# Optimization experiments

Measured on AMD Instinct MI355X. Metric: run time of the kernel, lower is better.

The kernel has to match this reference:

```python
import jax
import jax.numpy as jnp
from jax import lax
import numpy as np

VOCAB = 50000
EMBED = 300
HIDDEN = 256
BATCH = 64
SEQ = 256
FORGET_BIAS = 1.0


def setup_inputs() -> dict:
    key = jax.random.key(0)
    k = jax.random.split(key, 6)
    x_in = jax.random.randint(k[0], (BATCH, SEQ), 0, VOCAB, dtype=jnp.int64)
    embedding = jax.random.normal(k[1], (VOCAB, EMBED), dtype=jnp.float32)
    W0 = jax.random.normal(k[2], (EMBED + HIDDEN, 4 * HIDDEN), dtype=jnp.float32) * 0.05
    b0 = jnp.zeros((4 * HIDDEN,), dtype=jnp.float32)
    W1 = jax.random.normal(k[3], (HIDDEN + HIDDEN, 4 * HIDDEN), dtype=jnp.float32) * 0.05
    b1 = jnp.zeros((4 * HIDDEN,), dtype=jnp.float32)
    return {"x_in": x_in, "embedding": embedding, "W0": W0, "b0": b0, "W1": W1, "b1": b1}


def _lstm_layer(xs, W, b):
    # xs: [B, T, D] -> hidden sequence [B, T, H] (BasicLSTMCell, gate order i,j,f,o)
    B = xs.shape[0]
    H = W.shape[1] // 4

    def step(carry, x_t):
        c, h = carry
        gates = jnp.dot(jnp.concatenate([x_t, h], axis=-1), W) + b  # [B, 4H]
        i, j, f, o = jnp.split(gates, 4, axis=-1)
        new_c = c * jax.nn.sigmoid(f + FORGET_BIAS) + jax.nn.sigmoid(i) * jnp.tanh(j)
        new_h = jnp.tanh(new_c) * jax.nn.sigmoid(o)
        return (new_c, new_h), new_h

    init = (jnp.zeros((B, H), xs.dtype), jnp.zeros((B, H), xs.dtype))
    _, hs = lax.scan(step, init, jnp.swapaxes(xs, 0, 1))  # hs: [T, B, H]
    return jnp.swapaxes(hs, 0, 1)


def reference(x_in, embedding, W0, b0, W1, b1):
    word_vecs = embedding[x_in]                 # [B, T, E] frozen embedding lookup
    h1 = _lstm_layer(word_vecs, W0, b0)         # layer 1
    h2 = _lstm_layer(h1, W1, b1)                # layer 2
    return h2[:, -1, :]                          # output at last timestep [B, H]
```

## Files before the change

### kernel.cpp

```cpp
#include <hip/hip_runtime.h>

#define EMBED   300
#define HIDDEN  256
#define SEQ     256
#define NG      1024
#define EPOCHS  258

typedef __attribute__((ext_vector_type(8))) short  short8;
typedef __attribute__((ext_vector_type(4))) float  f32x4;
typedef __attribute__((ext_vector_type(2))) unsigned long long ull2;

__device__ inline unsigned short f2bf(float f) {
    unsigned u = __builtin_bit_cast(unsigned, f);
    return (unsigned short)((u + 0x7FFFu + ((u >> 16) & 1u)) >> 16);
}
__device__ inline float bf2f(unsigned short h) {
    unsigned u = (unsigned)h << 16;
    return __builtin_bit_cast(float, u);
}
__device__ inline float sigm(float x)  { return 1.0f / (1.0f + __expf(-x)); }
__device__ inline float tanh_(float x) { return 2.0f / (1.0f + __expf(-2.0f * x)) - 1.0f; }
__device__ inline int swzb(int c, int base) { return base ^ (((c >> 1) & 3) << 4); }

__device__ inline unsigned ld32a(const unsigned* p) {
    return __hip_atomic_load(p, __ATOMIC_RELAXED, __HIP_MEMORY_SCOPE_AGENT);
}
__device__ inline void st32a(unsigned* p, unsigned v) {
    __hip_atomic_store(p, v, __ATOMIC_RELAXED, __HIP_MEMORY_SCOPE_AGENT);
}
__device__ inline unsigned long long ld64a(const unsigned long long* p) {
    return __hip_atomic_load(p, __ATOMIC_RELAXED, __HIP_MEMORY_SCOPE_AGENT);
}
__device__ inline void st64a(unsigned long long* p, unsigned long long v) {
    __hip_atomic_store(p, v, __ATOMIC_RELAXED, __HIP_MEMORY_SCOPE_AGENT);
}
__device__ inline float ldf32a(const float* p) {
    return __builtin_bit_cast(float, ld32a((const unsigned*)p));
}
__device__ inline void stf32a(float* p, float v) {
    st32a((unsigned*)p, __builtin_bit_cast(unsigned, v));
}
__device__ inline short8 ldh16(const unsigned short* p) {
    ull2 t;
    t.x = ld64a((const unsigned long long*)p);
    t.y = ld64a((const unsigned long long*)p + 1);
    return __builtin_bit_cast(short8, t);
}

#define MFMA(a, b, c) __builtin_amdgcn_mfma_f32_16x16x32_bf16((a), (b), (c), 0, 0, 0)

template <bool FULL>
__global__ __launch_bounds__(256, 1) void lstm_fused(
    const int*   __restrict__ xin,
    const float* __restrict__ emb,
    const float* __restrict__ W0, const float* __restrict__ b0,
    const float* __restrict__ W1, const float* __restrict__ b1,
    unsigned*       __restrict__ flags,
    unsigned short* __restrict__ h1buf,
    unsigned short* __restrict__ h2buf,
    float*          __restrict__ ring1,
    float*          __restrict__ ring2,
    float*          __restrict__ out)
{
    extern __shared__ unsigned short lds[];
    const int tid = threadIdx.x, bid = blockIdx.x;
    const int w = tid >> 6, lane = tid & 63, l15 = lane & 15, q = lane >> 4;
    const int bbase = w * 16, arow = bbase + l15;

    int role, u0 = 0, hc0 = 0;
    if      (bid < 16) { role = 0; u0 = bid * 16; }
    else if (bid < 32) { role = 1; u0 = (bid - 16) * 16; }
    else if (FULL && bid < 48) { role = 2; u0 = (bid - 32) * 16; }
    else { role = 3; hc0 = (bid - (FULL ? 48 : 32)) * 32; }
    const int u = u0 + l15;

    if (bid < 16)       st64a((unsigned long long*)h1buf + bid * 256 + tid, 0ULL);
    else if (bid < 32)  st64a((unsigned long long*)h2buf + (bid - 16) * 256 + tid, 0ULL);

    short8 bfragR[8][4];
    float  bias_r[4];
    float  biasH[2];

    if (role == 0 || role == 1) {
        const float* Wl = role ? W1 : W0;
        const int    ro = role ? HIDDEN : EMBED;
        #pragma unroll
        for (int s = 0; s < 8; ++s)
            #pragma unroll
            for (int nt = 0; nt < 4; ++nt)
                #pragma unroll
                for (int e2 = 0; e2 < 8; ++e2) {
                    int k = ro + s * 32 + q * 8 + e2;
                    bfragR[s][nt][e2] = (short)f2bf(Wl[(long)k * NG + nt * 256 + u0 + l15]);
                }
    }
    if ((FULL && role == 2) || (!FULL && role == 1)) {
        #pragma unroll
        for (int nt = 0; nt < 4; ++nt) bias_r[nt] = b1[nt * 256 + u0 + l15];
        for (int idx = tid; idx < 8 * 64 * 32; idx += 256) {
            int k = idx >> 6, c = idx & 63;
            int col = (c >> 4) * 256 + u0 + (c & 15);
            int s = k >> 5, kk = k & 31;
            *(unsigned short*)((char*)lds + s * 4096 + swzb(c, c * 64 + kk * 2)) =
                f2bf(W1[(long)k * NG + col]);
        }
    }
    if (role == 3) {
        #pragma unroll
        for (int gi = 0; gi < 2; ++gi) biasH[gi] = b0[hc0 + gi * 16 + l15];
        for (int idx = tid; idx < 20 * 32 * 32; idx += 256) {
            int k = idx >> 5, c = idx & 31;
            int s = k >> 5, kk = k & 31;
            int row = (s >= 10) ? (k - 320) : k;
            float v = W0[(long)row * NG + hc0 + c];
            unsigned short hv = f2bf(v);
            if (s >= 10) hv = f2bf(v - bf2f(hv));
            *(unsigned short*)((char*)lds + s * 2048 + swzb(c, c * 64 + kk * 2)) = hv;
        }
    }
    __syncthreads();

    auto produce = [&](int t) {
        int xid = xin[arow * SEQ + t];
        const float* erow = emb + (long)xid * EMBED;
        short8 ac[10];
        #pragma unroll
        for (int s = 0; s < 10; ++s) {
            int kb = s * 32 + q * 8;
            #pragma unroll
            for (int hh = 0; hh < 2; ++hh) {
                int k4 = kb + hh * 4;
                if (k4 < EMBED) {
                    f32x4 v = *(const f32x4*)(erow + k4);
                    #pragma unroll
                    for (int e2 = 0; e2 < 4; ++e2) ac[s][hh * 4 + e2] = (short)f2bf(v[e2]);
                } else {
                    #pragma unroll
                    for (int e2 = 0; e2 < 4; ++e2) ac[s][hh * 4 + e2] = 0;
                }
            }
        }
        f32x4 accg[2];
        #pragma unroll
        for (int gi = 0; gi < 2; ++gi)
            accg[gi] = (f32x4){biasH[gi], biasH[gi], biasH[gi], biasH[gi]};
        #pragma unroll
        for (int s = 0; s < 20; ++s) {
            short8 a = ac[(s < 10) ? s : s - 10];
            #pragma unroll
            for (int gi = 0; gi < 2; ++gi) {
                int c = gi * 16 + l15;
                short8 b = *(const short8*)((char*)lds + s * 2048 + swzb(c, c * 64 + q * 16));
                accg[gi] = MFMA(a, b, accg[gi]);
            }
        }
        float* dst = ring1 + (long)(t & 3) * (64 * NG);
        #pragma unroll
        for (int gi = 0; gi < 2; ++gi)
            #pragma unroll
            for (int rr = 0; rr < 4; ++rr)
                stf32a(dst + (bbase + q * 4 + rr) * NG + hc0 + gi * 16 + l15, accg[gi][rr]);
    };

    if (role == 3) { produce(0); produce(1); produce(2); }

    bool alive = true;
    auto waitall = [&](unsigned tgt) {
        if (alive && w == 0) {
            int n = 0;
            for (;;) {
                unsigned v0 = ld32a(flags + lane * 16);
                unsigned v1 = 0xFFFFFFFFu;
                if (FULL && lane < 16) v1 = ld32a(flags + (64 + lane) * 16);
                if (__all((v0 >= tgt) && (v1 >= tgt))) break;
                if (++n > (1 << 17)) { alive = false; break; }
            }
        }
        __syncthreads();
    };

    asm volatile("s_waitcnt vmcnt(0)" ::: "memory");
    __syncthreads();
    if (tid == 0) { asm volatile("s_waitcnt vmcnt(0)" ::: "memory"); st32a(flags + bid * 16, 1u); }
    waitall(1u);

    float c4[4] = {0.f, 0.f, 0.f, 0.f};
    f32x4 gnext[4];
    f32x4 accx[4];

    if (role == 0) {
        #pragma unroll
        for (int nt = 0; nt < 4; ++nt)
            #pragma unroll
            for (int rr = 0; rr < 4; ++rr)
                gnext[nt][rr] = ldf32a(ring1 + (bbase + q * 4 + rr) * NG + nt * 256 + u0 + l15);
    }

    for (int e = 0; e < EPOCHS; ++e) {
        const int par_w = e & 1, par_r = (e - 1) & 1;

        const bool do_main = (role == 0 && e <= 255) || (role == 1 && e >= 2);
        if (do_main) {
            const unsigned short* hr = (role == 0 ? h1buf : h2buf) + par_r * 16384;
            f32x4 acc[4];
            if (role == 0) {
                #pragma unroll
                for (int nt = 0; nt < 4; ++nt) acc[nt] = gnext[nt];
            } else if (FULL) {
                const float* g2 = ring2 + (long)((e - 2) & 1) * (64 * NG);
                #pragma unroll
                for (int nt = 0; nt < 4; ++nt)
                    #pragma unroll
                    for (int rr = 0; rr < 4; ++rr)
                        acc[nt][rr] = ldf32a(g2 + (bbase + q * 4 + rr) * NG + nt * 256 + u0 + l15);
            } else {
                #pragma unroll
                for (int nt = 0; nt < 4; ++nt) acc[nt] = accx[nt];
            }
            short8 a8[8];
            #pragma unroll
            for (int s = 0; s < 8; ++s)
                a8[s] = ldh16(hr + arow * HIDDEN + s * 32 + q * 8);
            #pragma unroll
            for (int s = 0; s < 8; ++s)
                #pragma unroll
                for (int nt = 0; nt < 4; ++nt)
                    acc[nt] = MFMA(a8[s], bfragR[s][nt], acc[nt]);
            #pragma unroll
            for (int rr = 0; rr < 4; ++rr) {
                int b = bbase + q * 4 + rr;
                float iv = sigm(acc[0][rr]);
                float jv = tanh_(acc[1][rr]);
                float fv = sigm(acc[2][rr] + 1.0f);
                float ov = sigm(acc[3][rr]);
                float cn = c4[rr] * fv + iv * jv;
                c4[rr] = cn;
                float hn = tanh_(cn) * ov;
                *(unsigned short*)((char*)lds + 32768 + (b * 16 + l15) * 2) = f2bf(hn);
                if (role == 1 && e == 257) out[b * HIDDEN + u] = hn;
            }
        } else if (FULL && role == 2 && e >= 1 && e <= 256) {
            const int t = e - 1;
            const unsigned short* h1r = h1buf + (t & 1) * 16384;
            f32x4 g[4];
            #pragma unroll
            for (int nt = 0; nt < 4; ++nt)
                g[nt] = (f32x4){bias_r[nt], bias_r[nt], bias_r[nt], bias_r[nt]};
            #pragma unroll
            for (int s = 0; s < 8; ++s) {
                short8 a = ldh16(h1r + arow * HIDDEN + s * 32 + q * 8);
                #pragma unroll
                for (int nt = 0; nt < 4; ++nt) {
                    int c = nt * 16 + l15;
                    short8 b = *(const short8*)((char*)lds + s * 4096 + swzb(c, c * 64 + q * 16));
                    g[nt] = MFMA(a, b, g[nt]);
                }
            }
            float* dst = ring2 + (long)(t & 1) * (64 * NG);
            #pragma unroll
            for (int nt = 0; nt < 4; ++nt)
                #pragma unroll
                for (int rr = 0; rr < 4; ++rr)
                    stf32a(dst + (bbase + q * 4 + rr) * NG + nt * 256 + u0 + l15, g[nt][rr]);
        }

        __syncthreads();

        if (do_main) {
            unsigned short* hw = (role == 0 ? h1buf : h2buf) + par_w * 16384;
            unsigned long long v = *(unsigned long long*)((char*)lds + 32768 + tid * 8);
            int r = tid >> 2, p = tid & 3;
            st64a((unsigned long long*)(hw + r * HIDDEN + u0) + p, v);
        }
        asm volatile("s_waitcnt vmcnt(0)" ::: "memory");
        __syncthreads();
        if (tid == 0) { asm volatile("s_waitcnt vmcnt(0)" ::: "memory"); st32a(flags + bid * 16, (unsigned)(e + 2)); }

        if (role == 0 && e + 1 <= 255) {
            const float* g1 = ring1 + (long)((e + 1) & 3) * (64 * NG);
            #pragma unroll
            for (int nt = 0; nt < 4; ++nt)
                #pragma unroll
                for (int rr = 0; rr < 4; ++rr)
                    gnext[nt][rr] = ldf32a(g1 + (bbase + q * 4 + rr) * NG + nt * 256 + u0 + l15);
        } else if (!FULL && role == 1 && e >= 1 && e <= 256) {
            const unsigned short* h1r = h1buf + ((e - 1) & 1) * 16384;
            #pragma unroll
            for (int nt = 0; nt < 4; ++nt)
                accx[nt] = (f32x4){bias_r[nt], bias_r[nt], bias_r[nt], bias_r[nt]};
            #pragma unroll
            for (int s = 0; s < 8; ++s) {
                short8 a = ldh16(h1r + arow * HIDDEN + s * 32 + q * 8);
                #pragma unroll
                for (int nt = 0; nt < 4; ++nt) {
                    int c = nt * 16 + l15;
                    short8 b = *(const short8*)((char*)lds + s * 4096 + swzb(c, c * 64 + q * 16));
                    accx[nt] = MFMA(a, b, accx[nt]);
                }
            }
        } else if (role == 3 && e <= 252) {
            produce(e + 3);
        }

        waitall((unsigned)(e + 2));
    }
}

__global__ void ws_too_small_sentinel(float* out, int n) {
    int i = blockIdx.x * 256 + threadIdx.x;
    if (i < n) out[i] = 31337.0f;
}

extern "C" void kernel_launch(void* const* d_in, const int* in_sizes, int n_in,
                              void* d_out, int out_size, void* d_ws, size_t ws_size,
                              hipStream_t stream)
{
    const int*   xin = (const int*)d_in[0];
    const float* emb = (const float*)d_in[1];
    const float* W0  = (const float*)d_in[2];
    const float* b0  = (const float*)d_in[3];
    const float* W1  = (const float*)d_in[4];
    const float* b1  = (const float*)d_in[5];
    float* out = (float*)d_out;

    const size_t OFF_H1    = 0;
    const size_t OFF_H2    = OFF_H1 + 65536;
    const size_t OFF_RING1 = OFF_H2 + 65536;
    const size_t OFF_FLAGS = OFF_RING1 + (size_t)4 * 64 * NG * 4;
    const size_t NEED_FB   = OFF_FLAGS + 4096;
    const size_t OFF_RING2 = OFF_FLAGS + 8192;
    const size_t NEED_FULL = OFF_RING2 + (size_t)2 * 64 * NG * 4;

    if (ws_size < NEED_FB) {
        ws_too_small_sentinel<<<(out_size + 255) / 256, 256, 0, stream>>>(out, out_size);
        return;
    }
    const bool full = (ws_size >= NEED_FULL);

    char* ws = (char*)d_ws;
    unsigned short* h1buf = (unsigned short*)(ws + OFF_H1);
    unsigned short* h2buf = (unsigned short*)(ws + OFF_H2);
    float*          ring1 = (float*)(ws + OFF_RING1);
    unsigned*       flags = (unsigned*)(ws + OFF_FLAGS);
    float*          ring2 = full ? (float*)(ws + OFF_RING2) : ring1;

    hipMemsetAsync(flags, 0, full ? 8192 : 4096, stream);
    if (full) {
        lstm_fused<true><<<dim3(80), dim3(256), 40960, stream>>>(
            xin, emb, W0, b0, W1, b1, flags, h1buf, h2buf, ring1, ring2, out);
    } else {
        lstm_fused<false><<<dim3(64), dim3(256), 40960, stream>>>(
            xin, emb, W0, b0, W1, b1, flags, h1buf, h2buf, ring1, ring2, out);
    }
}
```

Measured before the change: 1.307 ms.

## Fuse both LSTM layers into 32 main blocks with point-to-point flag waits

Replaces the role-split persistent kernel with 32 main blocks that each own 8 hidden units of both layers, computing layer-1 and layer-2 recurrences plus the layer-2 input projection from register-resident bf16 weights. It also adds 32 producer blocks that precompute the embedding projection into a ring buffer, with backpressure. The global all-block barrier per epoch becomes targeted flag waits on only the dependencies each block needs, removing the separate ring2 path and templated fallback. It aims to cut per-step synchronisation latency, at the cost of more registers per main block and fewer blocks sharing the serial work.

```diff
diff --git a/kernel.cpp b/kernel.cpp
--- a/kernel.cpp
+++ b/kernel.cpp
@@ -4,11 +4,11 @@
 #define HIDDEN  256
 #define SEQ     256
 #define NG      1024
-#define EPOCHS  258
+#define NMAIN   32
+#define CAP     (1 << 17)
 
 typedef __attribute__((ext_vector_type(8))) short  short8;
 typedef __attribute__((ext_vector_type(4))) float  f32x4;
-typedef __attribute__((ext_vector_type(2))) unsigned long long ull2;
 
 __device__ inline unsigned short f2bf(float f) {
     unsigned u = __builtin_bit_cast(unsigned, f);
@@ -40,269 +40,284 @@
 __device__ inline void stf32a(float* p, float v) {
     st32a((unsigned*)p, __builtin_bit_cast(unsigned, v));
 }
-__device__ inline short8 ldh16(const unsigned short* p) {
-    ull2 t;
-    t.x = ld64a((const unsigned long long*)p);
-    t.y = ld64a((const unsigned long long*)p + 1);
-    return __builtin_bit_cast(short8, t);
+__device__ inline short8 ldh16a(const unsigned short* p) {
+    unsigned long long t0 = ld64a((const unsigned long long*)p);
+    unsigned long long t1 = ld64a((const unsigned long long*)p + 1);
+    union { unsigned long long q[2]; short8 s; } u;
+    u.q[0] = t0; u.q[1] = t1;
+    return u.s;
 }
 
 #define MFMA(a, b, c) __builtin_amdgcn_mfma_f32_16x16x32_bf16((a), (b), (c), 0, 0, 0)
 
-template <bool FULL>
-__global__ __launch_bounds__(256, 1) void lstm_fused(
+__global__ __launch_bounds__(256, 1) void lstm_v5(
     const int*   __restrict__ xin,
     const float* __restrict__ emb,
     const float* __restrict__ W0, const float* __restrict__ b0,
     const float* __restrict__ W1, const float* __restrict__ b1,
     unsigned*       __restrict__ flags,
-    unsigned short* __restrict__ h1buf,
-    unsigned short* __restrict__ h2buf,
+    unsigned short* __restrict__ h1,
+    unsigned short* __restrict__ h2,
     float*          __restrict__ ring1,
-    float*          __restrict__ ring2,
     float*          __restrict__ out)
 {
-    extern __shared__ unsigned short lds[];
+    extern __shared__ char lds[];
+    int* aliveP = (int*)(lds + 40960);
     const int tid = threadIdx.x, bid = blockIdx.x;
     const int w = tid >> 6, lane = tid & 63, l15 = lane & 15, q = lane >> 4;
     const int bbase = w * 16, arow = bbase + l15;
-
-    int role, u0 = 0, hc0 = 0;
-    if      (bid < 16) { role = 0; u0 = bid * 16; }
-    else if (bid < 32) { role = 1; u0 = (bid - 16) * 16; }
-    else if (FULL && bid < 48) { role = 2; u0 = (bid - 32) * 16; }
-    else { role = 3; hc0 = (bid - (FULL ? 48 : 32)) * 32; }
-    const int u = u0 + l15;
-
-    if (bid < 16)       st64a((unsigned long long*)h1buf + bid * 256 + tid, 0ULL);
-    else if (bid < 32)  st64a((unsigned long long*)h2buf + (bid - 16) * 256 + tid, 0ULL);
-
-    short8 bfragR[8][4];
-    float  bias_r[4];
-    float  biasH[2];
-
-    if (role == 0 || role == 1) {
-        const float* Wl = role ? W1 : W0;
-        const int    ro = role ? HIDDEN : EMBED;
+    bool alive = true;
+
+    if (bid < NMAIN) {
+        const int m = bid, u0 = m * 8;
+        const int lo8 = l15 & 7;
+        const bool gA = (l15 < 8);
+
+        if (tid < 128) {
+            int r = tid >> 1, p = tid & 1;
+            st64a((unsigned long long*)(h1 + 16384 + r * 256 + u0) + p, 0ULL);
+            st64a((unsigned long long*)(h2 +     0 + r * 256 + u0) + p, 0ULL);
+            st64a((unsigned long long*)(h2 + 16384 + r * 256 + u0) + p, 0ULL);
+        }
+
+        short8 bW0r[8][2], bW1x[8][2], bW1r[8][2];
+        float biasx[2];
         #pragma unroll
-        for (int s = 0; s < 8; ++s)
-            #pragma unroll
-            for (int nt = 0; nt < 4; ++nt)
+        for (int nt = 0; nt < 2; ++nt) {
+            int col = (2 * nt + (l15 >> 3)) * 256 + u0 + lo8;
+            biasx[nt] = b1[col];
+            #pragma unroll
+            for (int s = 0; s < 8; ++s)
                 #pragma unroll
                 for (int e2 = 0; e2 < 8; ++e2) {
-                    int k = ro + s * 32 + q * 8 + e2;
-                    bfragR[s][nt][e2] = (short)f2bf(Wl[(long)k * NG + nt * 256 + u0 + l15]);
-                }
-    }
-    if ((FULL && role == 2) || (!FULL && role == 1)) {
+                    int k = s * 32 + q * 8 + e2;
+                    bW0r[s][nt][e2] = (short)f2bf(W0[(long)(EMBED + k) * NG + col]);
+                    bW1x[s][nt][e2] = (short)f2bf(W1[(long)k * NG + col]);
+                    bW1r[s][nt][e2] = (short)f2bf(W1[(long)(HIDDEN + k) * NG + col]);
+                }
+        }
+        asm volatile("s_waitcnt vmcnt(0)" ::: "memory");
+        __syncthreads();
+        if (tid == 0) { st32a(flags + m * 16, 1u); st32a(flags + (32 + m) * 16, 1u); }
+
+        if (w == 0) {
+            int n = 0;
+            for (;;) {
+                unsigned hv = (lane < 32) ? ld32a(flags + (64 + lane) * 16) : 0xFFFFFFFFu;
+                if (__all(hv >= 1u)) break;
+                if (++n > CAP) { alive = false; stf32a(out, 51000.f); break; }
+            }
+        }
+        if (tid == 0) *aliveP = alive ? 1 : 0;
+        __syncthreads();
+        if (*aliveP == 0) return;
+
+        f32x4 gn[2];
         #pragma unroll
-        for (int nt = 0; nt < 4; ++nt) bias_r[nt] = b1[nt * 256 + u0 + l15];
-        for (int idx = tid; idx < 8 * 64 * 32; idx += 256) {
-            int k = idx >> 6, c = idx & 63;
-            int col = (c >> 4) * 256 + u0 + (c & 15);
-            int s = k >> 5, kk = k & 31;
-            *(unsigned short*)((char*)lds + s * 4096 + swzb(c, c * 64 + kk * 2)) =
-                f2bf(W1[(long)k * NG + col]);
-        }
-    }
-    if (role == 3) {
+        for (int nt = 0; nt < 2; ++nt) {
+            int col = (2 * nt + (l15 >> 3)) * 256 + u0 + lo8;
+            #pragma unroll
+            for (int rr = 0; rr < 4; ++rr)
+                gn[nt][rr] = ldf32a(ring1 + (size_t)(bbase + q * 4 + rr) * NG + col);
+        }
+
+        float c1[4] = {0.f, 0.f, 0.f, 0.f}, c2[4] = {0.f, 0.f, 0.f, 0.f};
+
+        for (int e = 0; e <= 256; ++e) {
+            if (w == 0) {
+                unsigned need = (lane < 32) ? (unsigned)(e + 1) : (unsigned)e;
+                const unsigned* fp = flags + lane * 16;
+                const bool nh = (e <= 254) && (lane < 32);
+                const unsigned* hp = flags + (64 + lane) * 16;
+                int n = 0;
+                for (;;) {
+                    unsigned v  = ld32a(fp);
+                    unsigned hv = nh ? ld32a(hp) : 0xFFFFFFFFu;
+                    if (__all((v >= need) && (hv >= (unsigned)(e + 2)))) break;
+                    if (++n > CAP) { alive = false; stf32a(out, 50000.f + (float)e); break; }
+                }
+            }
+            if (tid == 0) *aliveP = alive ? 1 : 0;
+            __syncthreads();
+            if (*aliveP == 0) break;
+
+            short8 a1[8], a2[8];
+            {
+                const unsigned short* p = h1 + ((e - 1) & 1) * 16384 + arow * 256;
+                #pragma unroll
+                for (int s = 0; s < 8; ++s) a1[s] = ldh16a(p + s * 32 + q * 8);
+            }
+            if (e >= 1) {
+                const unsigned short* p = h2 + (e & 1) * 16384 + arow * 256;
+                #pragma unroll
+                for (int s = 0; s < 8; ++s) a2[s] = ldh16a(p + s * 32 + q * 8);
+            }
+
+            f32x4 gacc[2];
+            if (e >= 1) {
+                #pragma unroll
+                for (int nt = 0; nt < 2; ++nt)
+                    gacc[nt] = (f32x4){biasx[nt], biasx[nt], biasx[nt], biasx[nt]};
+                #pragma unroll
+                for (int s = 0; s < 8; ++s)
+                    #pragma unroll
+                    for (int nt = 0; nt < 2; ++nt)
+                        gacc[nt] = MFMA(a1[s], bW1x[s][nt], gacc[nt]);
+            }
+
+            if (e <= 255) {
+                f32x4 acc[2] = {gn[0], gn[1]};
+                #pragma unroll
+                for (int s = 0; s < 8; ++s)
+                    #pragma unroll
+                    for (int nt = 0; nt < 2; ++nt)
+                        acc[nt] = MFMA(a1[s], bW0r[s][nt], acc[nt]);
+                #pragma unroll
+                for (int rr = 0; rr < 4; ++rr) {
+                    float x0 = acc[0][rr], x1 = acc[1][rr];
+                    float y0 = __shfl_xor(x0, 8), y1 = __shfl_xor(x1, 8);
+                    float iv = gA ? x0 : y0, jv = gA ? y0 : x0;
+                    float fv = gA ? x1 : y1, ov = gA ? y1 : x1;
+                    float cn = c1[rr] * sigm(fv + 1.f) + sigm(iv) * tanh_(jv);
+                    c1[rr] = cn;
+                    float hn = tanh_(cn) * sigm(ov);
+                    if (gA) *(unsigned short*)(lds + w * 256 + (q * 4 + rr) * 16 + lo8 * 2) = f2bf(hn);
+                }
+                asm volatile("s_waitcnt lgkmcnt(0)" ::: "memory");
+                if (q == 0) {
+                    unsigned long long v0 = *(unsigned long long*)(lds + w * 256 + l15 * 16);
+                    unsigned long long v1 = *(unsigned long long*)(lds + w * 256 + l15 * 16 + 8);
+                    unsigned long long* d = (unsigned long long*)(h1 + (e & 1) * 16384 + (bbase + l15) * 256 + u0);
+                    st64a(d, v0); st64a(d + 1, v1);
+                }
+            }
+            asm volatile("s_waitcnt vmcnt(0)" ::: "memory");
+            __syncthreads();
+            if (tid == 0 && e <= 255) st32a(flags + m * 16, (unsigned)(e + 2));
+
+            if (e <= 254) {
+                const float* g1 = ring1 + (size_t)((e + 1) & 3) * (64 * NG);
+                #pragma unroll
+                for (int nt = 0; nt < 2; ++nt) {
+                    int col = (2 * nt + (l15 >> 3)) * 256 + u0 + lo8;
+                    #pragma unroll
+                    for (int rr = 0; rr < 4; ++rr)
+                        gn[nt][rr] = ldf32a(g1 + (size_t)(bbase + q * 4 + rr) * NG + col);
+                }
+            }
+
+            if (e >= 1) {
+                f32x4 acc[2] = {gacc[0], gacc[1]};
+                #pragma unroll
+                for (int s = 0; s < 8; ++s)
+                    #pragma unroll
+                    for (int nt = 0; nt < 2; ++nt)
+                        acc[nt] = MFMA(a2[s], bW1r[s][nt], acc[nt]);
+                #pragma unroll
+                for (int rr = 0; rr < 4; ++rr) {
+                    float x0 = acc[0][rr], x1 = acc[1][rr];
+                    float y0 = __shfl_xor(x0, 8), y1 = __shfl_xor(x1, 8);
+                    float iv = gA ? x0 : y0, jv = gA ? y0 : x0;
+                    float fv = gA ? x1 : y1, ov = gA ? y1 : x1;
+                    float cn = c2[rr] * sigm(fv + 1.f) + sigm(iv) * tanh_(jv);
+                    c2[rr] = cn;
+                    float hn = tanh_(cn) * sigm(ov);
+                    if (e == 256) {
+                        if (gA) out[(bbase + q * 4 + rr) * 256 + u0 + lo8] = hn;
+                    } else {
+                        if (gA) *(unsigned short*)(lds + w * 256 + (q * 4 + rr) * 16 + lo8 * 2) = f2bf(hn);
+                    }
+                }
+                if (e < 256) {
+                    asm volatile("s_waitcnt lgkmcnt(0)" ::: "memory");
+                    if (q == 0) {
+                        unsigned long long v0 = *(unsigned long long*)(lds + w * 256 + l15 * 16);
+                        unsigned long long v1 = *(unsigned long long*)(lds + w * 256 + l15 * 16 + 8);
+                        unsigned long long* d = (unsigned long long*)(h2 + ((e - 1) & 1) * 16384 + (bbase + l15) * 256 + u0);
+                        st64a(d, v0); st64a(d + 1, v1);
+                    }
+                }
+            }
+            asm volatile("s_waitcnt vmcnt(0)" ::: "memory");
+            __syncthreads();
+            if (tid == 0 && e < 256) st32a(flags + (32 + m) * 16, (unsigned)(e + 2));
+        }
+
+    } else {
+        const int idx = bid - NMAIN;
+        const int hc0 = idx * 32;
+        float biasH[2];
         #pragma unroll
         for (int gi = 0; gi < 2; ++gi) biasH[gi] = b0[hc0 + gi * 16 + l15];
-        for (int idx = tid; idx < 20 * 32 * 32; idx += 256) {
-            int k = idx >> 5, c = idx & 31;
+        for (int i2 = tid; i2 < 20 * 32 * 32; i2 += 256) {
+            int k = i2 >> 5, c = i2 & 31;
             int s = k >> 5, kk = k & 31;
             int row = (s >= 10) ? (k - 320) : k;
             float v = W0[(long)row * NG + hc0 + c];
             unsigned short hv = f2bf(v);
             if (s >= 10) hv = f2bf(v - bf2f(hv));
-            *(unsigned short*)((char*)lds + s * 2048 + swzb(c, c * 64 + kk * 2)) = hv;
-        }
-    }
-    __syncthreads();
-
-    auto produce = [&](int t) {
-        int xid = xin[arow * SEQ + t];
-        const float* erow = emb + (long)xid * EMBED;
-        short8 ac[10];
-        #pragma unroll
-        for (int s = 0; s < 10; ++s) {
-            int kb = s * 32 + q * 8;
-            #pragma unroll
-            for (int hh = 0; hh < 2; ++hh) {
-                int k4 = kb + hh * 4;
-                if (k4 < EMBED) {
-                    f32x4 v = *(const f32x4*)(erow + k4);
-                    #pragma unroll
-                    for (int e2 = 0; e2 < 4; ++e2) ac[s][hh * 4 + e2] = (short)f2bf(v[e2]);
-                } else {
-                    #pragma unroll
-                    for (int e2 = 0; e2 < 4; ++e2) ac[s][hh * 4 + e2] = 0;
-                }
-            }
-        }
-        f32x4 accg[2];
-        #pragma unroll
-        for (int gi = 0; gi < 2; ++gi)
-            accg[gi] = (f32x4){biasH[gi], biasH[gi], biasH[gi], biasH[gi]};
-        #pragma unroll
-        for (int s = 0; s < 20; ++s) {
-            short8 a = ac[(s < 10) ? s : s - 10];
-            #pragma unroll
-            for (int gi = 0; gi < 2; ++gi) {
-                int c = gi * 16 + l15;
-                short8 b = *(const short8*)((char*)lds + s * 2048 + swzb(c, c * 64 + q * 16));
-                accg[gi] = MFMA(a, b, accg[gi]);
-            }
-        }
-        float* dst = ring1 + (long)(t & 3) * (64 * NG);
-        #pragma unroll
-        for (int gi = 0; gi < 2; ++gi)
-            #pragma unroll
-            for (int rr = 0; rr < 4; ++rr)
-                stf32a(dst + (bbase + q * 4 + rr) * NG + hc0 + gi * 16 + l15, accg[gi][rr]);
-    };
-
-    if (role == 3) { produce(0); produce(1); produce(2); }
-
-    bool alive = true;
-    auto waitall = [&](unsigned tgt) {
-        if (alive && w == 0) {
-            int n = 0;
-            for (;;) {
-                unsigned v0 = ld32a(flags + lane * 16);
-                unsigned v1 = 0xFFFFFFFFu;
-                if (FULL && lane < 16) v1 = ld32a(flags + (64 + lane) * 16);
-                if (__all((v0 >= tgt) && (v1 >= tgt))) break;
-                if (++n > (1 << 17)) { alive = false; break; }
-            }
+            *(unsigned short*)(lds + s * 2048 + swzb(c, c * 64 + kk * 2)) = hv;
         }
         __syncthreads();
-    };
-
-    asm volatile("s_waitcnt vmcnt(0)" ::: "memory");
-    __syncthreads();
-    if (tid == 0) { asm volatile("s_waitcnt vmcnt(0)" ::: "memory"); st32a(flags + bid * 16, 1u); }
-    waitall(1u);
-
-    float c4[4] = {0.f, 0.f, 0.f, 0.f};
-    f32x4 gnext[4];
-    f32x4 accx[4];
-
-    if (role == 0) {
-        #pragma unroll
-        for (int nt = 0; nt < 4; ++nt)
-            #pragma unroll
-            for (int rr = 0; rr < 4; ++rr)
-                gnext[nt][rr] = ldf32a(ring1 + (bbase + q * 4 + rr) * NG + nt * 256 + u0 + l15);
-    }
-
-    for (int e = 0; e < EPOCHS; ++e) {
-        const int par_w = e & 1, par_r = (e - 1) & 1;
-
-        const bool do_main = (role == 0 && e <= 255) || (role == 1 && e >= 2);
-        if (do_main) {
-            const unsigned short* hr = (role == 0 ? h1buf : h2buf) + par_r * 16384;
-            f32x4 acc[4];
-            if (role == 0) {
-                #pragma unroll
-                for (int nt = 0; nt < 4; ++nt) acc[nt] = gnext[nt];
-            } else if (FULL) {
-                const float* g2 = ring2 + (long)((e - 2) & 1) * (64 * NG);
-                #pragma unroll
-                for (int nt = 0; nt < 4; ++nt)
-                    #pragma unroll
-                    for (int rr = 0; rr < 4; ++rr)
-                        acc[nt][rr] = ldf32a(g2 + (bbase + q * 4 + rr) * NG + nt * 256 + u0 + l15);
-            } else {
-                #pragma unroll
-                for (int nt = 0; nt < 4; ++nt) acc[nt] = accx[nt];
-            }
-            short8 a8[8];
-            #pragma unroll
-            for (int s = 0; s < 8; ++s)
-                a8[s] = ldh16(hr + arow * HIDDEN + s * 32 + q * 8);
-            #pragma unroll
-            for (int s = 0; s < 8; ++s)
-                #pragma unroll
-                for (int nt = 0; nt < 4; ++nt)
-                    acc[nt] = MFMA(a8[s], bfragR[s][nt], acc[nt]);
-            #pragma unroll
-            for (int rr = 0; rr < 4; ++rr) {
-                int b = bbase + q * 4 + rr;
-                float iv = sigm(acc[0][rr]);
-                float jv = tanh_(acc[1][rr]);
-                float fv = sigm(acc[2][rr] + 1.0f);
-                float ov = sigm(acc[3][rr]);
-                float cn = c4[rr] * fv + iv * jv;
-                c4[rr] = cn;
-                float hn = tanh_(cn) * ov;
-                *(unsigned short*)((char*)lds + 32768 + (b * 16 + l15) * 2) = f2bf(hn);
-                if (role == 1 && e == 257) out[b * HIDDEN + u] = hn;
-            }
-        } else if (FULL && role == 2 && e >= 1 && e <= 256) {
-            const int t = e - 1;
-            const unsigned short* h1r = h1buf + (t & 1) * 16384;
-            f32x4 g[4];
-            #pragma unroll
-            for (int nt = 0; nt < 4; ++nt)
-                g[nt] = (f32x4){bias_r[nt], bias_r[nt], bias_r[nt], bias_r[nt]};
-            #pragma unroll
-            for (int s = 0; s < 8; ++s) {
-                short8 a = ldh16(h1r + arow * HIDDEN + s * 32 + q * 8);
-                #pragma unroll
-                for (int nt = 0; nt < 4; ++nt) {
-                    int c = nt * 16 + l15;
-                    short8 b = *(const short8*)((char*)lds + s * 4096 + swzb(c, c * 64 + q * 16));
-                    g[nt] = MFMA(a, b, g[nt]);
-                }
-            }
-            float* dst = ring2 + (long)(t & 1) * (64 * NG);
-            #pragma unroll
-            for (int nt = 0; nt < 4; ++nt)
+
+        for (int t = 0; t <= 255; ++t) {
+            int xid = xin[arow * SEQ + t];
+            const float* erow = emb + (long)xid * EMBED;
+            short8 ac[10];
+            #pragma unroll
+            for (int s = 0; s < 10; ++s) {
+                int kb = s * 32 + q * 8;
+                #pragma unroll
+                for (int hh = 0; hh < 2; ++hh) {
+                    int k4 = kb + hh * 4;
+                    if (k4 < EMBED) {
+                        f32x4 v = *(const f32x4*)(erow + k4);
+                        #pragma unroll
+                        for (int e2 = 0; e2 < 4; ++e2) ac[s][hh * 4 + e2] = (short)f2bf(v[e2]);
+                    } else {
+                        #pragma unroll
+                        for (int e2 = 0; e2 < 4; ++e2) ac[s][hh * 4 + e2] = 0;
+                    }
+                }
+            }
+            f32x4 accg[2];
+            #pragma unroll
+            for (int gi = 0; gi < 2; ++gi)
+                accg[gi] = (f32x4){biasH[gi], biasH[gi], biasH[gi], biasH[gi]};
+            #pragma unroll
+            for (int s = 0; s < 20; ++s) {
+                short8 a = ac[(s < 10) ? s : s - 10];
+                #pragma unroll
+                for (int gi = 0; gi < 2; ++gi) {
+                    int c = gi * 16 + l15;
+                    short8 b = *(const short8*)(lds + s * 2048 + swzb(c, c * 64 + q * 16));
+                    accg[gi] = MFMA(a, b, accg[gi]);
+                }
+            }
+            if (t >= 3) {
+                unsigned need = (t - 3 < 2) ? 2u : (unsigned)(t - 3);
+                if (w == 0) {
+                    int n = 0;
+                    for (;;) {
+                        unsigned v = (lane < 32) ? ld32a(flags + (32 + lane) * 16) : 0xFFFFFFFFu;
+                        if (__all(v >= need)) break;
+                        if (++n > CAP) { alive = false; stf32a(out + 1, 60000.f + (float)t); break; }
+                    }
+                }
+                if (tid == 0) *aliveP = alive ? 1 : 0;
+                __syncthreads();
+                if (*aliveP == 0) break;
+            }
+            float* dst = ring1 + (size_t)(t & 3) * (64 * NG);
+            #pragma unroll
+            for (int gi = 0; gi < 2; ++gi)
                 #pragma unroll
                 for (int rr = 0; rr < 4; ++rr)
-                    stf32a(dst + (bbase + q * 4 + rr) * NG + nt * 256 + u0 + l15, g[nt][rr]);
-        }
-
-        __syncthreads();
-
-        if (do_main) {
-            unsigned short* hw = (role == 0 ? h1buf : h2buf) + par_w * 16384;
-            unsigned long long v = *(unsigned long long*)((char*)lds + 32768 + tid * 8);
-            int r = tid >> 2, p = tid & 3;
-            st64a((unsigned long long*)(hw + r * HIDDEN + u0) + p, v);
-        }
-        asm volatile("s_waitcnt vmcnt(0)" ::: "memory");
-        __syncthreads();
-        if (tid == 0) { asm volatile("s_waitcnt vmcnt(0)" ::: "memory"); st32a(flags + bid * 16, (unsigned)(e + 2)); }
-
-        if (role == 0 && e + 1 <= 255) {
-            const float* g1 = ring1 + (long)((e + 1) & 3) * (64 * NG);
-            #pragma unroll
-            for (int nt = 0; nt < 4; ++nt)
-                #pragma unroll
-                for (int rr = 0; rr < 4; ++rr)
-                    gnext[nt][rr] = ldf32a(g1 + (bbase + q * 4 + rr) * NG + nt * 256 + u0 + l15);
-        } else if (!FULL && role == 1 && e >= 1 && e <= 256) {
-            const unsigned short* h1r = h1buf + ((e - 1) & 1) * 16384;
-            #pragma unroll
-            for (int nt = 0; nt < 4; ++nt)
-                accx[nt] = (f32x4){bias_r[nt], bias_r[nt], bias_r[nt], bias_r[nt]};
-            #pragma unroll
-            for (int s = 0; s < 8; ++s) {
-                short8 a = ldh16(h1r + arow * HIDDEN + s * 32 + q * 8);
-                #pragma unroll
-                for (int nt = 0; nt < 4; ++nt) {
-                    int c = nt * 16 + l15;
-                    short8 b = *(const short8*)((char*)lds + s * 4096 + swzb(c, c * 64 + q * 16));
-                    accx[nt] = MFMA(a, b, accx[nt]);
-                }
-            }
-        } else if (role == 3 && e <= 252) {
-            produce(e + 3);
-        }
-
-        waitall((unsigned)(e + 2));
+                    stf32a(dst + (size_t)(bbase + q * 4 + rr) * NG + hc0 + gi * 16 + l15, accg[gi][rr]);
+            asm volatile("s_waitcnt vmcnt(0)" ::: "memory");
+            __syncthreads();
+            if (tid == 0) st32a(flags + (64 + idx) * 16, (unsigned)(t + 1));
+        }
     }
 }
 
@@ -323,33 +338,24 @@
     const float* b1  = (const float*)d_in[5];
     float* out = (float*)d_out;
 
-    const size_t OFF_H1    = 0;
+    const size_t OFF_FLAGS = 0;
+    const size_t OFF_H1    = 8192;
     const size_t OFF_H2    = OFF_H1 + 65536;
     const size_t OFF_RING1 = OFF_H2 + 65536;
-    const size_t OFF_FLAGS = OFF_RING1 + (size_t)4 * 64 * NG * 4;
-    const size_t NEED_FB   = OFF_FLAGS + 4096;
-    const size_t OFF_RING2 = OFF_FLAGS + 8192;
-    const size_t NEED_FULL = OFF_RING2 + (size_t)2 * 64 * NG * 4;
-
-    if (ws_size < NEED_FB) {
+    const size_t NEED      = OFF_RING1 + (size_t)4 * 64 * NG * 4;
+
+    if (ws_size < NEED) {
         ws_too_small_sentinel<<<(out_size + 255) / 256, 256, 0, stream>>>(out, out_size);
         return;
     }
-    const bool full = (ws_size >= NEED_FULL);
 
     char* ws = (char*)d_ws;
-    unsigned short* h1buf = (unsigned short*)(ws + OFF_H1);
-    unsigned short* h2buf = (unsigned short*)(ws + OFF_H2);
+    unsigned*       flags = (unsigned*)(ws + OFF_FLAGS);
+    unsigned short* h1    = (unsigned short*)(ws + OFF_H1);
+    unsigned short* h2    = (unsigned short*)(ws + OFF_H2);
     float*          ring1 = (float*)(ws + OFF_RING1);
-    unsigned*       flags = (unsigned*)(ws + OFF_FLAGS);
-    float*          ring2 = full ? (float*)(ws + OFF_RING2) : ring1;
-
-    hipMemsetAsync(flags, 0, full ? 8192 : 4096, stream);
-    if (full) {
-        lstm_fused<true><<<dim3(80), dim3(256), 40960, stream>>>(
-            xin, emb, W0, b0, W1, b1, flags, h1buf, h2buf, ring1, ring2, out);
-    } else {
-        lstm_fused<false><<<dim3(64), dim3(256), 40960, stream>>>(
-            xin, emb, W0, b0, W1, b1, flags, h1buf, h2buf, ring1, ring2, out);
-    }
-}
+
+    hipMemsetAsync(flags, 0, 8192, stream);
+    lstm_v5<<<dim3(64), dim3(256), 41984, stream>>>(
+        xin, emb, W0, b0, W1, b1, flags, h1, h2, ring1, out);
+}
```

Result: slower. 1.959 ms (+49.9%).
